# Kernel optimization log

Hardware: AMD Instinct MI355X
Metric: run time of the kernel (lower is better)

The kernel has to match this reference:

```python
import jax, jax.numpy as jnp
import numpy as np

# Clos factorization for in=out=4096, middle_switch_multiplier=4:
BIN, B1, B2, B3, BOUT = 64, 64, 256, 64, 64
B, C, D = 2, 4096, 4096


def setup_inputs() -> dict:
    key = jax.random.key(0)
    ks = jax.random.split(key, 7)
    k = 1.0 / np.sqrt(D)
    x = jax.random.normal(ks[0], (B, C, D), dtype=jnp.float32)
    # kaiming_uniform(a=sqrt(5)) on [bin,b1,b2]-like tensors ~ uniform(-bound, bound)
    w1 = jax.random.uniform(ks[1], (BIN, B1, B2), jnp.float32, -k, k)
    w2 = jax.random.uniform(ks[2], (B1, B2, B3), jnp.float32, -k, k)
    w3 = jax.random.uniform(ks[3], (B2, B3, BOUT), jnp.float32, -k, k)
    bias1 = jax.random.uniform(ks[4], (B1,), jnp.float32, -k, k)
    bias2 = jax.random.uniform(ks[5], (B2,), jnp.float32, -k, k)
    bias3 = jax.random.uniform(ks[6], (B3,), jnp.float32, -k, k)
    return {"x": x, "w1": w1, "w2": w2, "w3": w3,
            "bias1": bias1, "bias2": bias2, "bias3": bias3}


def reference(x, w1, w2, w3, bias1, bias2, bias3):
    b, c, _ = x.shape
    h = x.reshape(b, c, BIN, B1)                      # [b,c,n=bin,r=b1]
    h = jnp.einsum('bcnr,nrm->bcmr', h, w1) + bias1   # [b,c,b2,b1] + bias over b1
    h = jnp.einsum('bcmr,rmn->bcnm', h, w2) + bias2   # [b,c,b3,b2] + bias over b2
    h = jnp.einsum('bcnm,mro->bcor', h, w3) + bias3   # [b,c,bout,b3] + bias over b3
    return h.reshape(b, c, -1)                        # [b,c,out_features]
```

## Files before the change

### kernel.cpp

```cpp
#include <hip/hip_runtime.h>
#include <stdint.h>
#include <stddef.h>

typedef __bf16 bf16_t;
typedef __bf16 bf16x8 __attribute__((ext_vector_type(8)));
typedef __bf16 bf16x4 __attribute__((ext_vector_type(4)));
typedef float f32x4 __attribute__((ext_vector_type(4)));

#define VMW(n) asm volatile("s_waitcnt vmcnt(" #n ")" ::: "memory")
#define LGKM0 asm volatile("s_waitcnt lgkmcnt(0)" ::: "memory")
#define CFENCE asm volatile("" ::: "memory")
#define RAWBAR              \
  do {                      \
    __builtin_amdgcn_s_barrier(); \
    CFENCE;                 \
  } while (0)

__device__ __forceinline__ void gload_lds16(const void* g, void* l) {
  __builtin_amdgcn_global_load_lds(
      (const __attribute__((address_space(1))) uint32_t*)g,
      (__attribute__((address_space(3))) uint32_t*)l, 16, 0, 0);
}

__global__ void prep1_k(const float* __restrict__ w2, const float* __restrict__ w3,
                        float* __restrict__ w2s, bf16_t* __restrict__ w3pt) {
  __shared__ float lds[64][65];
  const int b = blockIdx.x;
  const int t = threadIdx.x;
  if (b < 64) {
    const int r = b, m = t;
    const float4* p = (const float4*)(w2 + ((size_t)(r * 256 + m)) * 64);
    float s = 0.f;
#pragma unroll
    for (int i = 0; i < 16; ++i) {
      float4 v = p[i];
      s += (v.x + v.y) + (v.z + v.w);
    }
    w2s[r * 256 + m] = s;
    return;
  }
  const int b2 = b - 64;
  const int r = b2 & 63;
  const int mt = (b2 >> 6) * 64;
#pragma unroll
  for (int it = 0; it < 16; ++it) {
    int idx = t + it * 256;
    int ml = idx >> 6, o = idx & 63;
    lds[ml][o] = w3[(size_t)(mt + ml) * 4096 + r * 64 + o];
  }
  __syncthreads();
#pragma unroll
  for (int it = 0; it < 16; ++it) {
    int idx = t + it * 256;
    int o = idx >> 6, ml = idx & 63;
    w3pt[(size_t)(o * 64 + r) * 256 + mt + ml] = (bf16_t)lds[ml][o];
  }
}

__global__ void prep2_k(const float* __restrict__ w1, const float* __restrict__ w2s,
                        const float* __restrict__ bias1, const float* __restrict__ bias2,
                        bf16_t* __restrict__ w1t, float* __restrict__ c2) {
  __shared__ float lds[64][65];
  const int b = blockIdx.x;
  const int t = threadIdx.x;
  if (b == 256) {
    float s = 64.f * bias2[t];
#pragma unroll 8
    for (int r = 0; r < 64; ++r) s += bias1[r] * w2s[r * 256 + t];
    c2[t] = s;
    return;
  }
  const int k0 = (b >> 2) * 64;
  const int mt = (b & 3) * 64;
#pragma unroll
  for (int it = 0; it < 16; ++it) {
    int idx = t + it * 256;
    int kl = idx >> 6, ml = idx & 63;
    int k = k0 + kl;
    lds[kl][ml] = w1[(size_t)k * 256 + mt + ml] * w2s[(k & 63) * 256 + mt + ml];
  }
  __syncthreads();
#pragma unroll
  for (int it = 0; it < 16; ++it) {
    int idx = t + it * 256;
    int ml = idx >> 6, kl = idx & 63;
    w1t[(size_t)(mt + ml) * 4096 + k0 + kl] = (bf16_t)lds[kl][ml];
  }
}

__global__ __launch_bounds__(512, 2) void gemm1_k(
    const float* __restrict__ X, const bf16_t* __restrict__ W1T,
    bf16_t* __restrict__ S4) {
  __shared__ __align__(16) bf16_t lA[2][128 * 64];
  __shared__ __align__(16) bf16_t lB[2][256 * 64];
  const int tid = threadIdx.x;
  const int lane = tid & 63;
  const int wv = tid >> 6;
  const int bid = (int)blockIdx.x;
  const int xcd = bid & 7;
  const int rr = bid >> 3;
  const int mtile = xcd * 8 + (rr & 7);
  const int kh = rr >> 3;
  const size_t m0 = (size_t)mtile * 128;
  const int kbase = kh * 1024;
  const int wm = wv >> 2, wn = wv & 3;
  const int ar = tid >> 4;
  const int ac = tid & 15;

  f32x4 acc[4][4];
#pragma unroll
  for (int i = 0; i < 4; ++i)
#pragma unroll
    for (int j = 0; j < 4; ++j) acc[i][j] = (f32x4){0.f, 0.f, 0.f, 0.f};

  float4 aX[4], aY[4];

  auto issueA = [&](float4 (&dst)[4], int kt) {
#pragma unroll
    for (int p = 0; p < 4; ++p) {
      int row = ar + p * 32;
      dst[p] = *(const float4*)(X + (m0 + row) * 4096 + (size_t)(kbase + kt * 64 + ac * 4));
    }
  };
  auto writeA = [&](const float4 (&src)[4], int buf) {
#pragma unroll
    for (int p = 0; p < 4; ++p) {
      int row = ar + p * 32;
      int off = row * 128 + ((ac * 8) ^ ((row & 7) << 4));
      bf16x4 v;
      v[0] = (bf16_t)src[p].x;
      v[1] = (bf16_t)src[p].y;
      v[2] = (bf16_t)src[p].z;
      v[3] = (bf16_t)src[p].w;
      *(bf16x4*)((char*)(&lA[buf][0]) + off) = v;
    }
  };
  auto issueB = [&](int buf, int kt) {
#pragma unroll
    for (int i = 0; i < 4; ++i) {
      int row = wv * 32 + i * 8 + (lane >> 3);
      int srckb = ((lane & 7) * 16) ^ ((row & 7) << 4);
      const char* src = (const char*)W1T + (size_t)row * 8192 + (size_t)(kbase + kt * 64) * 2 + srckb;
      char* dst = (char*)(&lB[buf][0]) + (wv * 32 + i * 8) * 128;
      gload_lds16(src, dst);
    }
  };
  auto compute = [&](int buf) {
#pragma unroll
    for (int kk = 0; kk < 2; ++kk) {
      const int kb = kk * 64 + ((lane >> 4) * 16);
      bf16x8 af[4], bfr[4];
#pragma unroll
      for (int mf = 0; mf < 4; ++mf) {
        int row = wm * 64 + mf * 16 + (lane & 15);
        int off = row * 128 + (kb ^ ((row & 7) << 4));
        af[mf] = *(const bf16x8*)((const char*)(&lA[buf][0]) + off);
      }
#pragma unroll
      for (int nf = 0; nf < 4; ++nf) {
        int row = wn * 64 + nf * 16 + (lane & 15);
        int off = row * 128 + (kb ^ ((row & 7) << 4));
        bfr[nf] = *(const bf16x8*)((const char*)(&lB[buf][0]) + off);
      }
#pragma unroll
      for (int mf = 0; mf < 4; ++mf)
#pragma unroll
        for (int nf = 0; nf < 4; ++nf)
          acc[mf][nf] = __builtin_amdgcn_mfma_f32_16x16x32_bf16(af[mf], bfr[nf], acc[mf][nf], 0, 0, 0);
    }
  };

  issueB(0, 0);
  CFENCE;
  issueA(aX, 0);
  CFENCE;
  issueB(1, 1);
  CFENCE;
  issueA(aY, 1);
  CFENCE;
  VMW(8);
  writeA(aX, 0);
  LGKM0;
  RAWBAR;

#pragma unroll 1
  for (int t2 = 0; t2 < 14; t2 += 2) {
    compute(0);
    RAWBAR;
    issueB(0, t2 + 2);
    CFENCE;
    issueA(aX, t2 + 2);
    CFENCE;
    VMW(8);
    writeA(aY, 1);
    LGKM0;
    RAWBAR;
    compute(1);
    RAWBAR;
    issueB(1, t2 + 3);
    CFENCE;
    issueA(aY, t2 + 3);
    CFENCE;
    VMW(8);
    writeA(aX, 0);
    LGKM0;
    RAWBAR;
  }
  compute(0);
  RAWBAR;
  VMW(0);
  writeA(aY, 1);
  LGKM0;
  RAWBAR;
  compute(1);

#pragma unroll
  for (int nf = 0; nf < 4; ++nf) {
    int col = wn * 64 + nf * 16 + (lane & 15);
#pragma unroll
    for (int mf = 0; mf < 4; ++mf) {
#pragma unroll
      for (int q = 0; q < 4; ++q) {
        int row = wm * 64 + mf * 16 + (lane >> 4) * 4 + q;
        S4[(m0 + row) * 1024 + (size_t)(kh * 256 + col)] = (bf16_t)acc[mf][nf][q];
      }
    }
  }
}

__global__ __launch_bounds__(256) void reduce_k(
    const bf16_t* __restrict__ S4, const float* __restrict__ c2,
    bf16_t* __restrict__ S) {
  const int bid = (int)blockIdx.x;
  const int base = (bid & 7) * 1024 + (bid >> 3) * 8;
  const int t = threadIdx.x;
  const int row = base + (t >> 5);
  const int c8 = (t & 31) << 3;
  float s[8];
  float4 ca = *(const float4*)(c2 + c8);
  float4 cb = *(const float4*)(c2 + c8 + 4);
  s[0] = ca.x; s[1] = ca.y; s[2] = ca.z; s[3] = ca.w;
  s[4] = cb.x; s[5] = cb.y; s[6] = cb.z; s[7] = cb.w;
#pragma unroll
  for (int h = 0; h < 4; ++h) {
    bf16x8 v = *(const bf16x8*)(S4 + (size_t)row * 1024 + h * 256 + c8);
#pragma unroll
    for (int j = 0; j < 8; ++j) s[j] += (float)v[j];
  }
  bf16x8 o;
#pragma unroll
  for (int j = 0; j < 8; ++j) o[j] = (bf16_t)s[j];
  *(bf16x8*)(S + (size_t)row * 256 + c8) = o;
}

__global__ __launch_bounds__(512, 2) void gemm2_k(
    const bf16_t* __restrict__ S, const bf16_t* __restrict__ W3pT,
    const float* __restrict__ bias3, float* __restrict__ OUT) {
  __shared__ __align__(16) bf16_t lA[2][128 * 64];
  __shared__ __align__(16) bf16_t lB[2][256 * 64];
  const int tid = threadIdx.x;
  const int lane = tid & 63;
  const int wv = tid >> 6;
  const int bid = (int)blockIdx.x;
  const int xcd = bid & 7;
  const int rest = bid >> 3;
  const int mt = xcd * 8 + (rest >> 4);
  const int nt = rest & 15;
  const size_t m0 = (size_t)mt * 128;
  const int n0 = nt * 256;
  const int wm = wv >> 2, wn = wv & 3;

  f32x4 acc[4][4];
#pragma unroll
  for (int i = 0; i < 4; ++i)
#pragma unroll
    for (int j = 0; j < 4; ++j) acc[i][j] = (f32x4){0.f, 0.f, 0.f, 0.f};

  auto stage = [&](int buf, int kt) {
#pragma unroll
    for (int i = 0; i < 2; ++i) {
      int row = wv * 16 + i * 8 + (lane >> 3);
      int srckb = ((lane & 7) * 16) ^ ((row & 7) << 4);
      const char* srcA = (const char*)S + (m0 + row) * 512 + (size_t)(kt * 128) + srckb;
      char* dstA = (char*)(&lA[buf][0]) + (wv * 16 + i * 8) * 128;
      gload_lds16(srcA, dstA);
    }
#pragma unroll
    for (int i = 0; i < 4; ++i) {
      int row = wv * 32 + i * 8 + (lane >> 3);
      int srckb = ((lane & 7) * 16) ^ ((row & 7) << 4);
      const char* srcB = (const char*)W3pT + (size_t)(n0 + row) * 512 + (size_t)(kt * 128) + srckb;
      char* dstB = (char*)(&lB[buf][0]) + (wv * 32 + i * 8) * 128;
      gload_lds16(srcB, dstB);
    }
  };
  auto compute = [&](int buf) {
#pragma unroll
    for (int kk = 0; kk < 2; ++kk) {
      const int kb = kk * 64 + ((lane >> 4) * 16);
      bf16x8 af[4], bfr[4];
#pragma unroll
      for (int mf = 0; mf < 4; ++mf) {
        int row = wm * 64 + mf * 16 + (lane & 15);
        int off = row * 128 + (kb ^ ((row & 7) << 4));
        af[mf] = *(const bf16x8*)((const char*)(&lA[buf][0]) + off);
      }
#pragma unroll
      for (int nf = 0; nf < 4; ++nf) {
        int row = wn * 64 + nf * 16 + (lane & 15);
        int off = row * 128 + (kb ^ ((row & 7) << 4));
        bfr[nf] = *(const bf16x8*)((const char*)(&lB[buf][0]) + off);
      }
#pragma unroll
      for (int mf = 0; mf < 4; ++mf)
#pragma unroll
        for (int nf = 0; nf < 4; ++nf)
          acc[mf][nf] = __builtin_amdgcn_mfma_f32_16x16x32_bf16(af[mf], bfr[nf], acc[mf][nf], 0, 0, 0);
    }
  };

  stage(0, 0);
  CFENCE;
  stage(1, 1);
  CFENCE;
  VMW(6);
  RAWBAR;
  compute(0);
  RAWBAR;
  stage(0, 2);
  CFENCE;
  VMW(6);
  RAWBAR;
  compute(1);
  RAWBAR;
  stage(1, 3);
  CFENCE;
  VMW(6);
  RAWBAR;
  compute(0);
  RAWBAR;
  VMW(0);
  RAWBAR;
  compute(1);

#pragma unroll
  for (int nf = 0; nf < 4; ++nf) {
    int jcol = wn * 64 + nf * 16 + (lane & 15);
    float b3 = bias3[jcol & 63];
    int j = n0 + jcol;
#pragma unroll
    for (int mf = 0; mf < 4; ++mf) {
#pragma unroll
      for (int q = 0; q < 4; ++q) {
        size_t row = m0 + (size_t)(wm * 64 + mf * 16 + (lane >> 4) * 4 + q);
        OUT[row * 4096 + j] = acc[mf][nf][q] + b3;
      }
    }
  }
}

extern "C" void kernel_launch(void* const* d_in, const int* in_sizes, int n_in,
                              void* d_out, int out_size, void* d_ws, size_t ws_size,
                              hipStream_t stream) {
  (void)in_sizes; (void)n_in; (void)out_size; (void)ws_size;
  const float* x  = (const float*)d_in[0];
  const float* w1 = (const float*)d_in[1];
  const float* w2 = (const float*)d_in[2];
  const float* w3 = (const float*)d_in[3];
  const float* b1 = (const float*)d_in[4];
  const float* b2 = (const float*)d_in[5];
  const float* b3 = (const float*)d_in[6];
  float* out = (float*)d_out;
  char* ws = (char*)d_ws;

  float*  w2s  = (float*)(ws + 0);
  float*  c2   = (float*)(ws + 65536);
  bf16_t* w1t  = (bf16_t*)(ws + 69632);
  bf16_t* w3pt = (bf16_t*)(ws + 69632 + 2097152);
  bf16_t* S4   = (bf16_t*)(ws + 69632 + 2 * 2097152);
  bf16_t* S    = (bf16_t*)(ws + 69632 + 2 * 2097152 + 16777216);

  prep1_k<<<320, 256, 0, stream>>>(w2, w3, w2s, w3pt);
  prep2_k<<<257, 256, 0, stream>>>(w1, w2s, b1, b2, w1t, c2);
  gemm1_k<<<256, 512, 0, stream>>>(x, w1t, S4);
  reduce_k<<<1024, 256, 0, stream>>>(S4, c2, S);
  gemm2_k<<<1024, 512, 0, stream>>>(S, w3pt, b3, out);
}
```

Baseline: 104.6 us.

## Drop split-K in first GEMM, fuse bias reduction into its epilogue

The first GEMM changes from a split-K scheme (128-row tiles, 4 K-splits writing partial sums) to full-K 32-row tiles. The c2 bias is now added in the epilogue, so the separate reduce kernel and the partial-sum buffer go away. The prep kernels are also regrouped so the w2 row sums are computed first and the w1 and w3 transforms share one launch. The goal is to remove the partial-sum write and reread plus one kernel launch. The cost is much less B reuse per block: each block still streams the full 256-wide W1T for only 32 rows, and each wave holds a 32x32 tile with fewer MFMAs per LDS load.

Measured after the change: 128.6 us. +22.9%, slower.

```diff
diff --git a/kernel.cpp b/kernel.cpp
--- a/kernel.cpp
+++ b/kernel.cpp
@@ -22,125 +22,111 @@
       (__attribute__((address_space(3))) uint32_t*)l, 16, 0, 0);
 }
 
-__global__ void prep1_k(const float* __restrict__ w2, const float* __restrict__ w3,
-                        float* __restrict__ w2s, bf16_t* __restrict__ w3pt) {
+__global__ __launch_bounds__(256) void w2s_k(const float* __restrict__ w2,
+                                             float* __restrict__ w2s) {
+  const int r = blockIdx.x, m = threadIdx.x;
+  const float4* p = (const float4*)(w2 + ((size_t)(r * 256 + m)) * 64);
+  float s = 0.f;
+#pragma unroll
+  for (int i = 0; i < 16; ++i) {
+    float4 v = p[i];
+    s += (v.x + v.y) + (v.z + v.w);
+  }
+  w2s[r * 256 + m] = s;
+}
+
+__global__ __launch_bounds__(256) void prep_k(
+    const float* __restrict__ w1, const float* __restrict__ w3,
+    const float* __restrict__ w2s, const float* __restrict__ bias1,
+    const float* __restrict__ bias2, bf16_t* __restrict__ w1t,
+    bf16_t* __restrict__ w3pt, float* __restrict__ c2) {
   __shared__ float lds[64][65];
   const int b = blockIdx.x;
   const int t = threadIdx.x;
-  if (b < 64) {
-    const int r = b, m = t;
-    const float4* p = (const float4*)(w2 + ((size_t)(r * 256 + m)) * 64);
-    float s = 0.f;
-#pragma unroll
-    for (int i = 0; i < 16; ++i) {
-      float4 v = p[i];
-      s += (v.x + v.y) + (v.z + v.w);
-    }
-    w2s[r * 256 + m] = s;
-    return;
-  }
-  const int b2 = b - 64;
-  const int r = b2 & 63;
-  const int mt = (b2 >> 6) * 64;
-#pragma unroll
-  for (int it = 0; it < 16; ++it) {
-    int idx = t + it * 256;
-    int ml = idx >> 6, o = idx & 63;
-    lds[ml][o] = w3[(size_t)(mt + ml) * 4096 + r * 64 + o];
-  }
-  __syncthreads();
-#pragma unroll
-  for (int it = 0; it < 16; ++it) {
-    int idx = t + it * 256;
-    int o = idx >> 6, ml = idx & 63;
-    w3pt[(size_t)(o * 64 + r) * 256 + mt + ml] = (bf16_t)lds[ml][o];
-  }
-}
-
-__global__ void prep2_k(const float* __restrict__ w1, const float* __restrict__ w2s,
-                        const float* __restrict__ bias1, const float* __restrict__ bias2,
-                        bf16_t* __restrict__ w1t, float* __restrict__ c2) {
-  __shared__ float lds[64][65];
-  const int b = blockIdx.x;
-  const int t = threadIdx.x;
-  if (b == 256) {
+  if (b == 512) {
     float s = 64.f * bias2[t];
 #pragma unroll 8
     for (int r = 0; r < 64; ++r) s += bias1[r] * w2s[r * 256 + t];
     c2[t] = s;
     return;
   }
-  const int k0 = (b >> 2) * 64;
-  const int mt = (b & 3) * 64;
+  if (b < 256) {
+    const int k0 = (b >> 2) * 64;
+    const int mt = (b & 3) * 64;
+#pragma unroll
+    for (int it = 0; it < 16; ++it) {
+      int idx = t + it * 256;
+      int kl = idx >> 6, ml = idx & 63;
+      int k = k0 + kl;
+      lds[kl][ml] = w1[(size_t)k * 256 + mt + ml] * w2s[(k & 63) * 256 + mt + ml];
+    }
+    __syncthreads();
+#pragma unroll
+    for (int it = 0; it < 16; ++it) {
+      int idx = t + it * 256;
+      int ml = idx >> 6, kl = idx & 63;
+      w1t[(size_t)(mt + ml) * 4096 + k0 + kl] = (bf16_t)lds[kl][ml];
+    }
+    return;
+  }
+  const int b2 = b - 256;
+  const int r = b2 & 63;
+  const int mt = (b2 >> 6) * 64;
 #pragma unroll
   for (int it = 0; it < 16; ++it) {
     int idx = t + it * 256;
-    int kl = idx >> 6, ml = idx & 63;
-    int k = k0 + kl;
-    lds[kl][ml] = w1[(size_t)k * 256 + mt + ml] * w2s[(k & 63) * 256 + mt + ml];
+    int ml = idx >> 6, o = idx & 63;
+    lds[ml][o] = w3[(size_t)(mt + ml) * 4096 + r * 64 + o];
   }
   __syncthreads();
 #pragma unroll
   for (int it = 0; it < 16; ++it) {
     int idx = t + it * 256;
-    int ml = idx >> 6, kl = idx & 63;
-    w1t[(size_t)(mt + ml) * 4096 + k0 + kl] = (bf16_t)lds[kl][ml];
+    int o = idx >> 6, ml = idx & 63;
+    w3pt[(size_t)(o * 64 + r) * 256 + mt + ml] = (bf16_t)lds[ml][o];
   }
 }
 
 __global__ __launch_bounds__(512, 2) void gemm1_k(
     const float* __restrict__ X, const bf16_t* __restrict__ W1T,
-    bf16_t* __restrict__ S4) {
-  __shared__ __align__(16) bf16_t lA[2][128 * 64];
+    const float* __restrict__ c2, bf16_t* __restrict__ S) {
+  __shared__ __align__(16) bf16_t lA[2][32 * 64];
   __shared__ __align__(16) bf16_t lB[2][256 * 64];
   const int tid = threadIdx.x;
   const int lane = tid & 63;
   const int wv = tid >> 6;
   const int bid = (int)blockIdx.x;
-  const int xcd = bid & 7;
-  const int rr = bid >> 3;
-  const int mtile = xcd * 8 + (rr & 7);
-  const int kh = rr >> 3;
-  const size_t m0 = (size_t)mtile * 128;
-  const int kbase = kh * 1024;
-  const int wm = wv >> 2, wn = wv & 3;
+  const int mtile = (bid & 7) * 32 + (bid >> 3);
+  const size_t m0 = (size_t)mtile * 32;
   const int ar = tid >> 4;
   const int ac = tid & 15;
 
-  f32x4 acc[4][4];
-#pragma unroll
-  for (int i = 0; i < 4; ++i)
-#pragma unroll
-    for (int j = 0; j < 4; ++j) acc[i][j] = (f32x4){0.f, 0.f, 0.f, 0.f};
-
-  float4 aX[4], aY[4];
-
-  auto issueA = [&](float4 (&dst)[4], int kt) {
-#pragma unroll
-    for (int p = 0; p < 4; ++p) {
-      int row = ar + p * 32;
-      dst[p] = *(const float4*)(X + (m0 + row) * 4096 + (size_t)(kbase + kt * 64 + ac * 4));
-    }
-  };
-  auto writeA = [&](const float4 (&src)[4], int buf) {
-#pragma unroll
-    for (int p = 0; p < 4; ++p) {
-      int row = ar + p * 32;
-      int off = row * 128 + ((ac * 8) ^ ((row & 7) << 4));
-      bf16x4 v;
-      v[0] = (bf16_t)src[p].x;
-      v[1] = (bf16_t)src[p].y;
-      v[2] = (bf16_t)src[p].z;
-      v[3] = (bf16_t)src[p].w;
-      *(bf16x4*)((char*)(&lA[buf][0]) + off) = v;
-    }
+  f32x4 acc[2][2];
+#pragma unroll
+  for (int i = 0; i < 2; ++i)
+#pragma unroll
+    for (int j = 0; j < 2; ++j) acc[i][j] = (f32x4){0.f, 0.f, 0.f, 0.f};
+
+  float4 aX, aY;
+
+  auto issueA = [&](float4& dst, int kt) {
+    dst = *(const float4*)(X + (m0 + ar) * 4096 + (size_t)(kt * 64 + ac * 4));
+  };
+  auto writeA = [&](const float4& src, int buf) {
+    int off = ar * 128 + ((ac * 8) ^ ((ar & 7) << 4));
+    bf16x4 v;
+    v[0] = (bf16_t)src.x;
+    v[1] = (bf16_t)src.y;
+    v[2] = (bf16_t)src.z;
+    v[3] = (bf16_t)src.w;
+    *(bf16x4*)((char*)(&lA[buf][0]) + off) = v;
   };
   auto issueB = [&](int buf, int kt) {
 #pragma unroll
     for (int i = 0; i < 4; ++i) {
       int row = wv * 32 + i * 8 + (lane >> 3);
       int srckb = ((lane & 7) * 16) ^ ((row & 7) << 4);
-      const char* src = (const char*)W1T + (size_t)row * 8192 + (size_t)(kbase + kt * 64) * 2 + srckb;
+      const char* src = (const char*)W1T + (size_t)row * 8192 + (size_t)(kt * 64) * 2 + srckb;
       char* dst = (char*)(&lB[buf][0]) + (wv * 32 + i * 8) * 128;
       gload_lds16(src, dst);
     }
@@ -149,23 +135,23 @@
 #pragma unroll
     for (int kk = 0; kk < 2; ++kk) {
       const int kb = kk * 64 + ((lane >> 4) * 16);
-      bf16x8 af[4], bfr[4];
-#pragma unroll
-      for (int mf = 0; mf < 4; ++mf) {
-        int row = wm * 64 + mf * 16 + (lane & 15);
+      bf16x8 af[2], bfr[2];
+#pragma unroll
+      for (int mf = 0; mf < 2; ++mf) {
+        int row = mf * 16 + (lane & 15);
         int off = row * 128 + (kb ^ ((row & 7) << 4));
         af[mf] = *(const bf16x8*)((const char*)(&lA[buf][0]) + off);
       }
 #pragma unroll
-      for (int nf = 0; nf < 4; ++nf) {
-        int row = wn * 64 + nf * 16 + (lane & 15);
+      for (int nf = 0; nf < 2; ++nf) {
+        int row = wv * 32 + nf * 16 + (lane & 15);
         int off = row * 128 + (kb ^ ((row & 7) << 4));
         bfr[nf] = *(const bf16x8*)((const char*)(&lB[buf][0]) + off);
       }
 #pragma unroll
-      for (int mf = 0; mf < 4; ++mf)
-#pragma unroll
-        for (int nf = 0; nf < 4; ++nf)
+      for (int mf = 0; mf < 2; ++mf)
+#pragma unroll
+        for (int nf = 0; nf < 2; ++nf)
           acc[mf][nf] = __builtin_amdgcn_mfma_f32_16x16x32_bf16(af[mf], bfr[nf], acc[mf][nf], 0, 0, 0);
     }
   };
@@ -178,20 +164,20 @@
   CFENCE;
   issueA(aY, 1);
   CFENCE;
-  VMW(8);
+  VMW(5);
   writeA(aX, 0);
   LGKM0;
   RAWBAR;
 
 #pragma unroll 1
-  for (int t2 = 0; t2 < 14; t2 += 2) {
+  for (int t2 = 0; t2 < 62; t2 += 2) {
     compute(0);
     RAWBAR;
     issueB(0, t2 + 2);
     CFENCE;
     issueA(aX, t2 + 2);
     CFENCE;
-    VMW(8);
+    VMW(5);
     writeA(aY, 1);
     LGKM0;
     RAWBAR;
@@ -201,7 +187,7 @@
     CFENCE;
     issueA(aY, t2 + 3);
     CFENCE;
-    VMW(8);
+    VMW(5);
     writeA(aX, 0);
     LGKM0;
     RAWBAR;
@@ -215,42 +201,18 @@
   compute(1);
 
 #pragma unroll
-  for (int nf = 0; nf < 4; ++nf) {
-    int col = wn * 64 + nf * 16 + (lane & 15);
-#pragma unroll
-    for (int mf = 0; mf < 4; ++mf) {
+  for (int nf = 0; nf < 2; ++nf) {
+    int col = wv * 32 + nf * 16 + (lane & 15);
+    float cadd = c2[col];
+#pragma unroll
+    for (int mf = 0; mf < 2; ++mf) {
 #pragma unroll
       for (int q = 0; q < 4; ++q) {
-        int row = wm * 64 + mf * 16 + (lane >> 4) * 4 + q;
-        S4[(m0 + row) * 1024 + (size_t)(kh * 256 + col)] = (bf16_t)acc[mf][nf][q];
-      }
-    }
-  }
-}
-
-__global__ __launch_bounds__(256) void reduce_k(
-    const bf16_t* __restrict__ S4, const float* __restrict__ c2,
-    bf16_t* __restrict__ S) {
-  const int bid = (int)blockIdx.x;
-  const int base = (bid & 7) * 1024 + (bid >> 3) * 8;
-  const int t = threadIdx.x;
-  const int row = base + (t >> 5);
-  const int c8 = (t & 31) << 3;
-  float s[8];
-  float4 ca = *(const float4*)(c2 + c8);
-  float4 cb = *(const float4*)(c2 + c8 + 4);
-  s[0] = ca.x; s[1] = ca.y; s[2] = ca.z; s[3] = ca.w;
-  s[4] = cb.x; s[5] = cb.y; s[6] = cb.z; s[7] = cb.w;
-#pragma unroll
-  for (int h = 0; h < 4; ++h) {
-    bf16x8 v = *(const bf16x8*)(S4 + (size_t)row * 1024 + h * 256 + c8);
-#pragma unroll
-    for (int j = 0; j < 8; ++j) s[j] += (float)v[j];
-  }
-  bf16x8 o;
-#pragma unroll
-  for (int j = 0; j < 8; ++j) o[j] = (bf16_t)s[j];
-  *(bf16x8*)(S + (size_t)row * 256 + c8) = o;
+        int row = mf * 16 + (lane >> 4) * 4 + q;
+        S[(m0 + row) * 256 + (size_t)col] = (bf16_t)(acc[mf][nf][q] + cadd);
+      }
+    }
+  }
 }
 
 __global__ __launch_bounds__(512, 2) void gemm2_k(
@@ -377,12 +339,10 @@
   float*  c2   = (float*)(ws + 65536);
   bf16_t* w1t  = (bf16_t*)(ws + 69632);
   bf16_t* w3pt = (bf16_t*)(ws + 69632 + 2097152);
-  bf16_t* S4   = (bf16_t*)(ws + 69632 + 2 * 2097152);
-  bf16_t* S    = (bf16_t*)(ws + 69632 + 2 * 2097152 + 16777216);
-
-  prep1_k<<<320, 256, 0, stream>>>(w2, w3, w2s, w3pt);
-  prep2_k<<<257, 256, 0, stream>>>(w1, w2s, b1, b2, w1t, c2);
-  gemm1_k<<<256, 512, 0, stream>>>(x, w1t, S4);
-  reduce_k<<<1024, 256, 0, stream>>>(S4, c2, S);
+  bf16_t* S    = (bf16_t*)(ws + 69632 + 2 * 2097152);
+
+  w2s_k<<<64, 256, 0, stream>>>(w2, w2s);
+  prep_k<<<513, 256, 0, stream>>>(w1, w3, w2s, b1, b2, w1t, w3pt, c2);
+  gemm1_k<<<256, 512, 0, stream>>>(x, w1t, c2, S);
   gemm2_k<<<1024, 512, 0, stream>>>(S, w3pt, b3, out);
 }
```
